# Performance work log

Measured on AMD Instinct MI355X. Metric: run time of the kernel, lower is better.

Reference implementation:

```python
import jax, jax.numpy as jnp
import numpy as np
from jax import lax

SIGMA_RATIO = 1.0 / 2.355
NUM_BINS = 32


def _correlation_ratio(pred, target, num_bins=NUM_BINS, sigma_ratio=SIGMA_RATIO):
    # Mirrors CorrRatio.correlation_ratio(pred, target).
    eps = jnp.finfo(target.dtype).eps
    # Quantile bounds are .item()'d in torch -> constants w.r.t. autodiff.
    f_max = lax.stop_gradient(jnp.quantile(target, 0.99))
    f_min = lax.stop_gradient(jnp.quantile(target, 0.01))
    m_max = lax.stop_gradient(jnp.quantile(pred, 0.99))
    m_min = lax.stop_gradient(jnp.quantile(pred, 0.01))

    f_bin_size = (f_max - f_min) / num_bins
    vbc = jnp.linspace(f_min + f_bin_size / 2, f_max - f_bin_size / 2, num_bins)  # (nb,)
    f_sigma = jnp.mean(jnp.diff(vbc)) * sigma_ratio
    preterm = 1.0 / (2.0 * f_sigma ** 2)

    B, C = target.shape[0], target.shape[1]
    y = jnp.clip(target, f_min, f_max).reshape(B, C, -1)  # (B,C,N)
    x = jnp.clip(pred, m_min, m_max).reshape(B, C, -1)    # (B,C,N)

    # Parzen-window weights: (B,C,nb,N)
    diff = y[:, :, None, :] - vbc[None, None, :, None]
    weights = jnp.exp(-preterm * jnp.square(diff))
    # Note: torch code normalizes over the voxel axis (dim=-1 == N).
    weights_norm = weights / (jnp.sum(weights, axis=-1, keepdims=True) + eps)

    mean_intensities = jnp.sum(weights_norm * x[:, :, None, :], axis=3)  # (B,C,nb)
    bin_counts = jnp.sum(weights, axis=3)                                # (B,C,nb)
    total_mean = jnp.mean(x, axis=2, keepdims=True)                      # (B,C,1)

    between_group_variance = jnp.sum(
        bin_counts * jnp.square(mean_intensities - total_mean), axis=2
    ) / (jnp.sum(bin_counts, axis=2) + eps)                              # (B,C)
    total_variance = jnp.var(x, axis=2, ddof=1)  # torch.var default: unbiased
    eta_square = between_group_variance / (total_variance + eps)
    return jnp.mean(eta_square)


def setup_inputs() -> dict:
    key = jax.random.key(0)
    k1, k2 = jax.random.split(key)
    shape = (1, 1, 128, 128, 128)
    y_true = jax.random.normal(k1, shape, dtype=jnp.float32)
    y_pred = jax.random.normal(k2, shape, dtype=jnp.float32)
    return {"y_true": y_true, "y_pred": y_pred}


def reference(y_true, y_pred):
    # forward: correlation_ratio(y_true, y_pred) maps to (pred=y_true, target=y_pred)
    symmetric_cr = _correlation_ratio(y_true, y_pred) + _correlation_ratio(y_pred, y_true)
    return -symmetric_cr / 2.0
```

## Files before the change

### kernel.cpp

```cpp
#include <hip/hip_runtime.h>
#include <stdint.h>

#define N_ELEM (128*128*128)
#define NBINS 32
#define CAP 32768
#define REPS 8
#define PBUF 1024

static constexpr size_t OFF_H12  = 0;
static constexpr size_t OFF_B12  = OFF_H12 + 2ull*4096ull*4ull;
static constexpr size_t OFF_R12  = OFF_B12 + 8*4;
static constexpr size_t OFF_CNT  = OFF_R12 + 8*4;
static constexpr size_t OFF_SEL  = OFF_CNT + 8*4;
static constexpr size_t OFF_ACC  = (OFF_SEL + 8*4 + 7) & ~size_t(7);
static constexpr size_t OFF_CAND = OFF_ACC + (size_t)REPS*2*66*8;
static constexpr size_t OFF_MEMSET_END = OFF_CAND;

__device__ __forceinline__ uint32_t f2k(float x){
    uint32_t b = __float_as_uint(x);
    return (b & 0x80000000u) ? ~b : (b | 0x80000000u);
}
__device__ __forceinline__ float k2f(uint32_t k){
    uint32_t b = (k & 0x80000000u) ? (k & 0x7FFFFFFFu) : ~k;
    return __uint_as_float(b);
}

__device__ __forceinline__ float fexp2(float x){
#if __has_builtin(__builtin_amdgcn_exp2f)
    return __builtin_amdgcn_exp2f(x);
#else
    return __expf(x * 0.6931471805599453f);
#endif
}

__global__ void __launch_bounds__(256) k_p1(const float* __restrict__ a0,
                                            const float* __restrict__ a1,
                                            uint32_t* __restrict__ hist12){
    __shared__ uint32_t lh[4096];
    for (int i = threadIdx.x; i < 4096; i += 256) lh[i] = 0;
    __syncthreads();
    const float4* s4 = (const float4*)(blockIdx.y ? a1 : a0);
    const int stride = gridDim.x * blockDim.x;
    for (int i = blockIdx.x * blockDim.x + threadIdx.x; i < N_ELEM/4; i += stride){
        float4 v = s4[i];
        atomicAdd(&lh[f2k(v.x) >> 20], 1u);
        atomicAdd(&lh[f2k(v.y) >> 20], 1u);
        atomicAdd(&lh[f2k(v.z) >> 20], 1u);
        atomicAdd(&lh[f2k(v.w) >> 20], 1u);
    }
    __syncthreads();
    uint32_t* gh = hist12 + (size_t)blockIdx.y * 4096u;
    for (int i = threadIdx.x; i < 4096; i += 256){
        uint32_t c = lh[i];
        if (c) atomicAdd(&gh[i], c);
    }
}

__global__ void __launch_bounds__(256) k_s1(const uint32_t* __restrict__ hist12,
                                            uint32_t* __restrict__ bucket12,
                                            uint32_t* __restrict__ resid12){
    __shared__ uint32_t part[256];
    const uint32_t R[4] = {20971u, 20972u, 2076179u, 2076180u};
    const int a = blockIdx.x;
    const int t = threadIdx.x;
    const uint4* h4 = (const uint4*)(hist12 + (size_t)a * 4096u);
    uint32_t v[16];
    uint32_t s = 0;
    #pragma unroll
    for (int j = 0; j < 4; ++j){
        uint4 q4 = h4[t*4 + j];
        v[j*4+0] = q4.x; v[j*4+1] = q4.y; v[j*4+2] = q4.z; v[j*4+3] = q4.w;
        s += q4.x + q4.y + q4.z + q4.w;
    }
    part[t] = s;
    __syncthreads();
    for (int d = 1; d < 256; d <<= 1){
        uint32_t add = (t >= d) ? part[t - d] : 0u;
        __syncthreads();
        part[t] += add;
        __syncthreads();
    }
    uint32_t c = part[t] - s;
    #pragma unroll
    for (int j = 0; j < 16; ++j){
        uint32_t cnt = v[j];
        if (cnt){
            for (int ri = 0; ri < 4; ++ri){
                uint32_t r = R[ri];
                if (r >= c && r < c + cnt){
                    bucket12[a*4 + ri] = (uint32_t)(t*16 + j);
                    resid12 [a*4 + ri] = r - c;
                }
            }
        }
        c += cnt;
    }
}

__global__ void __launch_bounds__(256) k_p2(const float* __restrict__ a0,
                                            const float* __restrict__ a1,
                                            const uint32_t* __restrict__ bucket12,
                                            uint32_t* __restrict__ cnt,
                                            float* __restrict__ cand){
    __shared__ uint32_t lcnt[4];
    __shared__ uint32_t gbase[4];
    __shared__ float lbuf[4][PBUF];
    const int t = threadIdx.x;
    const int base = blockIdx.y * 4;
    const uint32_t b0 = bucket12[base+0], b1 = bucket12[base+1];
    const uint32_t b2 = bucket12[base+2], b3 = bucket12[base+3];
    const bool own1 = (b1 != b0);
    const bool own2 = (b2 != b0) && (b2 != b1);
    const bool own3 = (b3 != b0) && (b3 != b1) && (b3 != b2);
    if (t < 4) lcnt[t] = 0;
    __syncthreads();
    const float4* s4 = (const float4*)(blockIdx.y ? a1 : a0);
    const int stride = gridDim.x * blockDim.x;
    for (int i = blockIdx.x * blockDim.x + t; i < N_ELEM/4; i += stride){
        float4 v = s4[i];
        float vv[4] = {v.x, v.y, v.z, v.w};
        #pragma unroll
        for (int e = 0; e < 4; ++e){
            uint32_t hi = f2k(vv[e]) >> 20;
            if (hi == b0){
                uint32_t x = atomicAdd(&lcnt[0], 1u);
                if (x < PBUF) lbuf[0][x] = vv[e];
                else { uint32_t g = atomicAdd(&cnt[base+0], 1u); if (g < CAP) cand[(size_t)(base+0)*CAP + g] = vv[e]; }
            }
            if (own1 && hi == b1){
                uint32_t x = atomicAdd(&lcnt[1], 1u);
                if (x < PBUF) lbuf[1][x] = vv[e];
                else { uint32_t g = atomicAdd(&cnt[base+1], 1u); if (g < CAP) cand[(size_t)(base+1)*CAP + g] = vv[e]; }
            }
            if (own2 && hi == b2){
                uint32_t x = atomicAdd(&lcnt[2], 1u);
                if (x < PBUF) lbuf[2][x] = vv[e];
                else { uint32_t g = atomicAdd(&cnt[base+2], 1u); if (g < CAP) cand[(size_t)(base+2)*CAP + g] = vv[e]; }
            }
            if (own3 && hi == b3){
                uint32_t x = atomicAdd(&lcnt[3], 1u);
                if (x < PBUF) lbuf[3][x] = vv[e];
                else { uint32_t g = atomicAdd(&cnt[base+3], 1u); if (g < CAP) cand[(size_t)(base+3)*CAP + g] = vv[e]; }
            }
        }
    }
    __syncthreads();
    if (t == 0){
        #pragma unroll
        for (int j = 0; j < 4; ++j){
            uint32_t n = min(lcnt[j], (uint32_t)PBUF);
            gbase[j] = n ? atomicAdd(&cnt[base+j], n) : 0u;
        }
    }
    __syncthreads();
    #pragma unroll
    for (int j = 0; j < 4; ++j){
        uint32_t n = min(lcnt[j], (uint32_t)PBUF);
        for (uint32_t i = t; i < n; i += 256){
            uint32_t g = gbase[j] + i;
            if (g < CAP) cand[(size_t)(base+j)*CAP + g] = lbuf[j][i];
        }
    }
}

__global__ void __launch_bounds__(256) k_s2(const float* __restrict__ cand,
                                            const uint32_t* __restrict__ cnt,
                                            const uint32_t* __restrict__ bucket12,
                                            const uint32_t* __restrict__ resid12,
                                            float* __restrict__ selval){
    __shared__ uint32_t lh[1024];
    __shared__ uint32_t part[256];
    __shared__ uint32_t sb_sh, r2_sh;
    const int r = blockIdx.x;
    const int t = threadIdx.x;
    const int base4 = (r >> 2) << 2;
    int o = base4;
    for (int i = base4; i <= r; ++i){
        if (bucket12[i] == bucket12[r]){ o = i; break; }
    }
    const uint32_t n = min(cnt[o], (uint32_t)CAP);
    const float* cb = cand + (size_t)o * CAP;
    const uint32_t rr = resid12[r];
    const uint32_t b12 = bucket12[r];

    for (int i = t; i < 1024; i += 256) lh[i] = 0;
    __syncthreads();
    for (uint32_t i = t; i < n; i += 256) atomicAdd(&lh[(f2k(cb[i]) >> 10) & 1023u], 1u);
    __syncthreads();
    {
        uint32_t v[4]; uint32_t s = 0;
        #pragma unroll
        for (int j = 0; j < 4; ++j){ v[j] = lh[t*4 + j]; s += v[j]; }
        part[t] = s;
        __syncthreads();
        for (int d = 1; d < 256; d <<= 1){
            uint32_t add = (t >= d) ? part[t - d] : 0u;
            __syncthreads();
            part[t] += add;
            __syncthreads();
        }
        uint32_t c = part[t] - s;
        #pragma unroll
        for (int j = 0; j < 4; ++j){
            if (v[j] && rr >= c && rr < c + v[j]){ sb_sh = (uint32_t)(t*4 + j); r2_sh = rr - c; }
            c += v[j];
        }
    }
    __syncthreads();
    const uint32_t sb = sb_sh, r2 = r2_sh;
    __syncthreads();

    for (int i = t; i < 1024; i += 256) lh[i] = 0;
    __syncthreads();
    for (uint32_t i = t; i < n; i += 256){
        uint32_t k = f2k(cb[i]);
        if (((k >> 10) & 1023u) == sb) atomicAdd(&lh[k & 1023u], 1u);
    }
    __syncthreads();
    {
        uint32_t v[4]; uint32_t s = 0;
        #pragma unroll
        for (int j = 0; j < 4; ++j){ v[j] = lh[t*4 + j]; s += v[j]; }
        part[t] = s;
        __syncthreads();
        for (int d = 1; d < 256; d <<= 1){
            uint32_t add = (t >= d) ? part[t - d] : 0u;
            __syncthreads();
            part[t] += add;
            __syncthreads();
        }
        uint32_t c = part[t] - s;
        #pragma unroll
        for (int j = 0; j < 4; ++j){
            if (v[j] && r2 >= c && r2 < c + v[j]){
                uint32_t key = (b12 << 20) | (sb << 10) | (uint32_t)(t*4 + j);
                selval[r] = k2f(key);
            }
            c += v[j];
        }
    }
}

__device__ __forceinline__ float wred(float v){
    #pragma unroll
    for (int o = 32; o > 0; o >>= 1) v += __shfl_down(v, o);
    return v;
}

__global__ void __launch_bounds__(128) k_main(const float* __restrict__ yt,
                                              const float* __restrict__ yp,
                                              const float* __restrict__ selval,
                                              double* __restrict__ acc){
    __shared__ float lp1[NBINS][128];
    __shared__ float lp2[NBINS][128];
    __shared__ float qs[4];
    const int t = threadIdx.x;
    const int dir = blockIdx.y;
    #pragma unroll
    for (int k = 0; k < NBINS; ++k){ lp1[k][t] = 0.f; lp2[k][t] = 0.f; }
    if (t == 0){
        double f01 = 0.01 * (double)(N_ELEM - 1) - 20971.0;
        double f99 = 0.99 * (double)(N_ELEM - 1) - 2076179.0;
        double v0 = selval[0], v1 = selval[1], v2 = selval[2], v3 = selval[3];
        double v4 = selval[4], v5 = selval[5], v6 = selval[6], v7 = selval[7];
        qs[0] = (float)(v0 + f01 * (v1 - v0));
        qs[1] = (float)(v2 + f99 * (v3 - v2));
        qs[2] = (float)(v4 + f01 * (v5 - v4));
        qs[3] = (float)(v6 + f99 * (v7 - v6));
    }
    __syncthreads();

    const float f_min = dir ? qs[0] : qs[2];
    const float f_max = dir ? qs[1] : qs[3];
    const float m_min = dir ? qs[2] : qs[0];
    const float m_max = dir ? qs[3] : qs[1];

    const float h      = (f_max - f_min) / 32.0f;
    const float vbc0   = f_min + 0.5f * h;
    const float vbcE   = f_max - 0.5f * h;
    const float step   = (vbcE - vbc0) / 31.0f;
    const float sigma  = step * (1.0f / 2.355f);
    const float preterm= 1.0f / (2.0f * sigma * sigma);
    const float negq2  = -preterm * step * step * 1.4426950408889634f;
    const float inv_st = 1.0f / step;
    const float u0     = -vbc0 * inv_st;

    const float4* ysrc = (const float4*)(dir ? yt : yp);
    const float4* xsrc = (const float4*)(dir ? yp : yt);

    float sx = 0.f, sxx = 0.f;
    const int stride = gridDim.x * blockDim.x;
    for (int i = blockIdx.x * blockDim.x + t; i < N_ELEM/4; i += stride){
        float4 y4 = ysrc[i];
        float4 x4 = xsrc[i];
        float yy[4] = {y4.x, y4.y, y4.z, y4.w};
        float xx[4] = {x4.x, x4.y, x4.z, x4.w};
        #pragma unroll
        for (int e = 0; e < 4; ++e){
            float yc = fminf(fmaxf(yy[e], f_min), f_max);
            float xc = fminf(fmaxf(xx[e], m_min), m_max);
            sx += xc; sxx = fmaf(xc, xc, sxx);
            float u  = fmaf(yc, inv_st, u0);
            float jf = fminf(fmaxf(floorf(u) - 2.0f, 0.0f), 26.0f);
            int j0 = (int)jf;
            float t0 = u - jf;
            float* p1 = &lp1[j0][t];
            float* p2 = &lp2[j0][t];
            #pragma unroll
            for (int w = 0; w < 6; ++w){
                float d  = t0 - (float)w;
                float wt = fexp2(d * d * negq2);
                p1[w*128] += wt;
                p2[w*128] += wt * xc;
            }
        }
    }
    __syncthreads();

    if (t < 64){
        #pragma unroll
        for (int k = 0; k < NBINS; ++k){ lp1[k][t] += lp1[k][t+64]; lp2[k][t] += lp2[k][t+64]; }
    }
    __syncthreads();
    if (t < 32){
        #pragma unroll
        for (int k = 0; k < NBINS; ++k){ lp1[k][t] += lp1[k][t+32]; lp2[k][t] += lp2[k][t+32]; }
    }
    __syncthreads();

    const int rep = blockIdx.x & (REPS - 1);
    double* a = acc + ((size_t)rep*2 + dir) * 66;
    if (t < 64){
        int arr = t >> 5, bin = t & 31;
        float s = 0.f;
        #pragma unroll
        for (int c = 0; c < 32; ++c){
            int cc = (c + t) & 31;
            s += arr ? lp2[bin][cc] : lp1[bin][cc];
        }
        atomicAdd(&a[t], (double)s);
    }
    sx = wred(sx); sxx = wred(sxx);
    if ((t & 63) == 0){
        atomicAdd(&a[64], (double)sx);
        atomicAdd(&a[65], (double)sxx);
    }
}

__global__ void __launch_bounds__(256) k_final(const double* __restrict__ acc,
                                               float* __restrict__ out){
    __shared__ double dA[132];
    const int t = threadIdx.x;
    if (t < 132){
        int dir = t / 66, k = t % 66;
        double s = 0.0;
        #pragma unroll
        for (int rep = 0; rep < REPS; ++rep) s += acc[((size_t)rep*2 + dir)*66 + k];
        dA[t] = s;
    }
    __syncthreads();
    if (t == 0){
        const double eps = 1.1920928955078125e-07;
        double res = 0.0;
        for (int dir = 0; dir < 2; ++dir){
            const double* A = &dA[dir*66];
            double sx = A[64], sxx = A[65];
            double tm = sx / (double)N_ELEM;
            double sumS1 = 0.0, bgv = 0.0;
            for (int k = 0; k < NBINS; ++k) sumS1 += A[k];
            for (int k = 0; k < NBINS; ++k){
                double mi = A[32+k] / (A[k] + eps);
                double d  = mi - tm;
                bgv += A[k] * d * d;
            }
            bgv /= (sumS1 + eps);
            double tv = (sxx - sx*sx/(double)N_ELEM) / (double)(N_ELEM - 1);
            res += bgv / (tv + eps);
        }
        out[0] = (float)(-0.5 * res);
    }
}

extern "C" void kernel_launch(void* const* d_in, const int* in_sizes, int n_in,
                              void* d_out, int out_size, void* d_ws, size_t ws_size,
                              hipStream_t stream){
    const float* yt = (const float*)d_in[0];
    const float* yp = (const float*)d_in[1];
    char* ws = (char*)d_ws;
    uint32_t* hist12   = (uint32_t*)(ws + OFF_H12);
    uint32_t* bucket12 = (uint32_t*)(ws + OFF_B12);
    uint32_t* resid12  = (uint32_t*)(ws + OFF_R12);
    uint32_t* cnt      = (uint32_t*)(ws + OFF_CNT);
    float*    selval   = (float*)(ws + OFF_SEL);
    double*   acc      = (double*)(ws + OFF_ACC);
    float*    cand     = (float*)(ws + OFF_CAND);

    hipMemsetAsync(d_ws, 0, OFF_MEMSET_END, stream);

    k_p1  <<<dim3(256, 2), 256, 0, stream>>>(yt, yp, hist12);
    k_s1  <<<2, 256, 0, stream>>>(hist12, bucket12, resid12);
    k_p2  <<<dim3(128, 2), 256, 0, stream>>>(yt, yp, bucket12, cnt, cand);
    k_s2  <<<8, 256, 0, stream>>>(cand, cnt, bucket12, resid12, selval);
    k_main<<<dim3(512, 2), 128, 0, stream>>>(yt, yp, selval, acc);
    k_final<<<1, 256, 0, stream>>>(acc, (float*)d_out);
}
```

Before: 92.74 us.

## Fuse scan and final kernels via last-block tickets, register-accumulate all 32 bins

Replaces the memset with a small zeroing kernel and folds the histogram-scan kernel into k_p1 and the final reduction into k_main, using an atomic ticket so the last block does the tail work. This removes launches. k_main now evaluates all 32 Gaussian bins per voxel in registers with wave shuffles instead of the windowed 6-tap shared-memory scatter. That drops LDS traffic but multiplies exp work by about 5x, and k_main moves to 256-thread blocks with half the grid.

Result: slower. 159.0 us (+71.4%).

```diff
diff --git a/kernel.cpp b/kernel.cpp
--- a/kernel.cpp
+++ b/kernel.cpp
@@ -6,15 +6,20 @@
 #define CAP 32768
 #define REPS 8
 #define PBUF 1024
-
-static constexpr size_t OFF_H12  = 0;
-static constexpr size_t OFF_B12  = OFF_H12 + 2ull*4096ull*4ull;
-static constexpr size_t OFF_R12  = OFF_B12 + 8*4;
-static constexpr size_t OFF_CNT  = OFF_R12 + 8*4;
-static constexpr size_t OFF_SEL  = OFF_CNT + 8*4;
-static constexpr size_t OFF_ACC  = (OFF_SEL + 8*4 + 7) & ~size_t(7);
-static constexpr size_t OFF_CAND = OFF_ACC + (size_t)REPS*2*66*8;
-static constexpr size_t OFF_MEMSET_END = OFF_CAND;
+#define GX_P1 256
+#define GX_P2 128
+#define GX_MAIN 256
+
+static constexpr size_t OFF_H12 = 0;
+static constexpr size_t OFF_CNT = OFF_H12 + 2ull*4096*4;
+static constexpr size_t OFF_TK  = OFF_CNT + 8*4;
+static constexpr size_t OFF_B12 = OFF_TK + 2*4;
+static constexpr size_t OFF_R12 = OFF_B12 + 8*4;
+static constexpr size_t OFF_SEL = OFF_R12 + 8*4;
+static constexpr size_t OFF_ACC = OFF_SEL + 8*4;
+static constexpr size_t OFF_ACC_END = OFF_ACC + (size_t)REPS*2*66*8;
+static constexpr size_t OFF_CAND = OFF_ACC_END;
+static constexpr int ZERO_WORDS = (int)(OFF_ACC_END / 4);
 
 __device__ __forceinline__ uint32_t f2k(float x){
     uint32_t b = __float_as_uint(x);
@@ -24,7 +29,6 @@
     uint32_t b = (k & 0x80000000u) ? (k & 0x7FFFFFFFu) : ~k;
     return __uint_as_float(b);
 }
-
 __device__ __forceinline__ float fexp2(float x){
 #if __has_builtin(__builtin_amdgcn_exp2f)
     return __builtin_amdgcn_exp2f(x);
@@ -32,16 +36,33 @@
     return __expf(x * 0.6931471805599453f);
 #endif
 }
+__device__ __forceinline__ float wred(float v){
+    #pragma unroll
+    for (int o = 32; o > 0; o >>= 1) v += __shfl_down(v, o);
+    return v;
+}
+
+__global__ void __launch_bounds__(256) k_zero(uint32_t* __restrict__ w){
+    const int stride = gridDim.x * blockDim.x;
+    for (int i = blockIdx.x * blockDim.x + threadIdx.x; i < ZERO_WORDS; i += stride)
+        w[i] = 0u;
+}
 
 __global__ void __launch_bounds__(256) k_p1(const float* __restrict__ a0,
                                             const float* __restrict__ a1,
-                                            uint32_t* __restrict__ hist12){
+                                            uint32_t* __restrict__ hist12,
+                                            uint32_t* __restrict__ ticket,
+                                            uint32_t* __restrict__ bucket12,
+                                            uint32_t* __restrict__ resid12){
     __shared__ uint32_t lh[4096];
-    for (int i = threadIdx.x; i < 4096; i += 256) lh[i] = 0;
+    __shared__ uint32_t part[256];
+    __shared__ uint32_t lastflag;
+    const int t = threadIdx.x;
+    for (int i = t; i < 4096; i += 256) lh[i] = 0;
     __syncthreads();
     const float4* s4 = (const float4*)(blockIdx.y ? a1 : a0);
-    const int stride = gridDim.x * blockDim.x;
-    for (int i = blockIdx.x * blockDim.x + threadIdx.x; i < N_ELEM/4; i += stride){
+    const int stride = GX_P1 * 256;
+    for (int i = blockIdx.x * 256 + t; i < N_ELEM/4; i += stride){
         float4 v = s4[i];
         atomicAdd(&lh[f2k(v.x) >> 20], 1u);
         atomicAdd(&lh[f2k(v.y) >> 20], 1u);
@@ -50,50 +71,47 @@
     }
     __syncthreads();
     uint32_t* gh = hist12 + (size_t)blockIdx.y * 4096u;
-    for (int i = threadIdx.x; i < 4096; i += 256){
+    for (int i = t; i < 4096; i += 256){
         uint32_t c = lh[i];
         if (c) atomicAdd(&gh[i], c);
     }
-}
-
-__global__ void __launch_bounds__(256) k_s1(const uint32_t* __restrict__ hist12,
-                                            uint32_t* __restrict__ bucket12,
-                                            uint32_t* __restrict__ resid12){
-    __shared__ uint32_t part[256];
+    __threadfence();
+    __syncthreads();
+    if (t == 0) lastflag = (atomicAdd(&ticket[0], 1u) == gridDim.x * gridDim.y - 1) ? 1u : 0u;
+    __syncthreads();
+    if (!lastflag) return;
+    __threadfence();
+
     const uint32_t R[4] = {20971u, 20972u, 2076179u, 2076180u};
-    const int a = blockIdx.x;
-    const int t = threadIdx.x;
-    const uint4* h4 = (const uint4*)(hist12 + (size_t)a * 4096u);
-    uint32_t v[16];
-    uint32_t s = 0;
-    #pragma unroll
-    for (int j = 0; j < 4; ++j){
-        uint4 q4 = h4[t*4 + j];
-        v[j*4+0] = q4.x; v[j*4+1] = q4.y; v[j*4+2] = q4.z; v[j*4+3] = q4.w;
-        s += q4.x + q4.y + q4.z + q4.w;
-    }
-    part[t] = s;
-    __syncthreads();
-    for (int d = 1; d < 256; d <<= 1){
-        uint32_t add = (t >= d) ? part[t - d] : 0u;
+    for (int a = 0; a < 2; ++a){
+        uint32_t* h = hist12 + (size_t)a * 4096u;
+        uint32_t v[16]; uint32_t s = 0;
+        #pragma unroll
+        for (int j = 0; j < 16; ++j){ v[j] = atomicAdd(&h[t*16 + j], 0u); s += v[j]; }
+        part[t] = s;
         __syncthreads();
-        part[t] += add;
+        for (int d = 1; d < 256; d <<= 1){
+            uint32_t add = (t >= d) ? part[t - d] : 0u;
+            __syncthreads();
+            part[t] += add;
+            __syncthreads();
+        }
+        uint32_t c = part[t] - s;
+        #pragma unroll
+        for (int j = 0; j < 16; ++j){
+            uint32_t cnt = v[j];
+            if (cnt){
+                for (int ri = 0; ri < 4; ++ri){
+                    uint32_t r = R[ri];
+                    if (r >= c && r < c + cnt){
+                        bucket12[a*4 + ri] = (uint32_t)(t*16 + j);
+                        resid12 [a*4 + ri] = r - c;
+                    }
+                }
+            }
+            c += cnt;
+        }
         __syncthreads();
-    }
-    uint32_t c = part[t] - s;
-    #pragma unroll
-    for (int j = 0; j < 16; ++j){
-        uint32_t cnt = v[j];
-        if (cnt){
-            for (int ri = 0; ri < 4; ++ri){
-                uint32_t r = R[ri];
-                if (r >= c && r < c + cnt){
-                    bucket12[a*4 + ri] = (uint32_t)(t*16 + j);
-                    resid12 [a*4 + ri] = r - c;
-                }
-            }
-        }
-        c += cnt;
     }
 }
 
@@ -115,8 +133,8 @@
     if (t < 4) lcnt[t] = 0;
     __syncthreads();
     const float4* s4 = (const float4*)(blockIdx.y ? a1 : a0);
-    const int stride = gridDim.x * blockDim.x;
-    for (int i = blockIdx.x * blockDim.x + t; i < N_ELEM/4; i += stride){
+    const int stride = GX_P2 * 256;
+    for (int i = blockIdx.x * 256 + t; i < N_ELEM/4; i += stride){
         float4 v = s4[i];
         float vv[4] = {v.x, v.y, v.z, v.w};
         #pragma unroll
@@ -241,23 +259,18 @@
     }
 }
 
-__device__ __forceinline__ float wred(float v){
-    #pragma unroll
-    for (int o = 32; o > 0; o >>= 1) v += __shfl_down(v, o);
-    return v;
-}
-
-__global__ void __launch_bounds__(128) k_main(const float* __restrict__ yt,
+__global__ void __launch_bounds__(256) k_main(const float* __restrict__ yt,
                                               const float* __restrict__ yp,
                                               const float* __restrict__ selval,
-                                              double* __restrict__ acc){
-    __shared__ float lp1[NBINS][128];
-    __shared__ float lp2[NBINS][128];
+                                              double* __restrict__ acc,
+                                              uint32_t* __restrict__ ticket,
+                                              float* __restrict__ out){
     __shared__ float qs[4];
+    __shared__ float wp[4][66];
+    __shared__ uint32_t lastflag;
+    __shared__ double dA[132];
     const int t = threadIdx.x;
     const int dir = blockIdx.y;
-    #pragma unroll
-    for (int k = 0; k < NBINS; ++k){ lp1[k][t] = 0.f; lp2[k][t] = 0.f; }
     if (t == 0){
         double f01 = 0.01 * (double)(N_ELEM - 1) - 20971.0;
         double f99 = 0.99 * (double)(N_ELEM - 1) - 2076179.0;
@@ -288,9 +301,13 @@
     const float4* ysrc = (const float4*)(dir ? yt : yp);
     const float4* xsrc = (const float4*)(dir ? yp : yt);
 
+    float s1[NBINS], s2[NBINS];
+    #pragma unroll
+    for (int k = 0; k < NBINS; ++k){ s1[k] = 0.f; s2[k] = 0.f; }
     float sx = 0.f, sxx = 0.f;
-    const int stride = gridDim.x * blockDim.x;
-    for (int i = blockIdx.x * blockDim.x + t; i < N_ELEM/4; i += stride){
+
+    const int stride = GX_MAIN * 256;
+    for (int i = blockIdx.x * 256 + t; i < N_ELEM/4; i += stride){
         float4 y4 = ysrc[i];
         float4 x4 = xsrc[i];
         float yy[4] = {y4.x, y4.y, y4.z, y4.w};
@@ -301,71 +318,54 @@
             float xc = fminf(fmaxf(xx[e], m_min), m_max);
             sx += xc; sxx = fmaf(xc, xc, sxx);
             float u  = fmaf(yc, inv_st, u0);
-            float jf = fminf(fmaxf(floorf(u) - 2.0f, 0.0f), 26.0f);
-            int j0 = (int)jf;
-            float t0 = u - jf;
-            float* p1 = &lp1[j0][t];
-            float* p2 = &lp2[j0][t];
             #pragma unroll
-            for (int w = 0; w < 6; ++w){
-                float d  = t0 - (float)w;
-                float wt = fexp2(d * d * negq2);
-                p1[w*128] += wt;
-                p2[w*128] += wt * xc;
-            }
-        }
-    }
-    __syncthreads();
-
-    if (t < 64){
-        #pragma unroll
-        for (int k = 0; k < NBINS; ++k){ lp1[k][t] += lp1[k][t+64]; lp2[k][t] += lp2[k][t+64]; }
-    }
-    __syncthreads();
-    if (t < 32){
-        #pragma unroll
-        for (int k = 0; k < NBINS; ++k){ lp1[k][t] += lp1[k][t+32]; lp2[k][t] += lp2[k][t+32]; }
-    }
-    __syncthreads();
-
+            for (int k = 0; k < NBINS; ++k){
+                float du = u - (float)k;
+                float w  = fexp2(negq2 * du * du);
+                s1[k] += w;
+                s2[k] = fmaf(w, xc, s2[k]);
+            }
+        }
+    }
+
+    #pragma unroll
+    for (int k = 0; k < NBINS; ++k){ s1[k] = wred(s1[k]); s2[k] = wred(s2[k]); }
+    sx = wred(sx); sxx = wred(sxx);
+    const int lane = t & 63, wave = t >> 6;
+    if (lane == 0){
+        #pragma unroll
+        for (int k = 0; k < NBINS; ++k){ wp[wave][k] = s1[k]; wp[wave][32+k] = s2[k]; }
+        wp[wave][64] = sx; wp[wave][65] = sxx;
+    }
+    __syncthreads();
     const int rep = blockIdx.x & (REPS - 1);
     double* a = acc + ((size_t)rep*2 + dir) * 66;
-    if (t < 64){
-        int arr = t >> 5, bin = t & 31;
-        float s = 0.f;
-        #pragma unroll
-        for (int c = 0; c < 32; ++c){
-            int cc = (c + t) & 31;
-            s += arr ? lp2[bin][cc] : lp1[bin][cc];
-        }
-        atomicAdd(&a[t], (double)s);
-    }
-    sx = wred(sx); sxx = wred(sxx);
-    if ((t & 63) == 0){
-        atomicAdd(&a[64], (double)sx);
-        atomicAdd(&a[65], (double)sxx);
-    }
-}
-
-__global__ void __launch_bounds__(256) k_final(const double* __restrict__ acc,
-                                               float* __restrict__ out){
-    __shared__ double dA[132];
-    const int t = threadIdx.x;
+    if (t < 66){
+        float v = wp[0][t] + wp[1][t] + wp[2][t] + wp[3][t];
+        atomicAdd(&a[t], (double)v);
+    }
+    __threadfence();
+    __syncthreads();
+    if (t == 0) lastflag = (atomicAdd(&ticket[1], 1u) == gridDim.x * gridDim.y - 1) ? 1u : 0u;
+    __syncthreads();
+    if (!lastflag) return;
+    __threadfence();
+
     if (t < 132){
-        int dir = t / 66, k = t % 66;
+        int d2 = t / 66, k = t % 66;
         double s = 0.0;
         #pragma unroll
-        for (int rep = 0; rep < REPS; ++rep) s += acc[((size_t)rep*2 + dir)*66 + k];
+        for (int r2 = 0; r2 < REPS; ++r2) s += atomicAdd(&acc[((size_t)r2*2 + d2)*66 + k], 0.0);
         dA[t] = s;
     }
     __syncthreads();
     if (t == 0){
         const double eps = 1.1920928955078125e-07;
         double res = 0.0;
-        for (int dir = 0; dir < 2; ++dir){
-            const double* A = &dA[dir*66];
-            double sx = A[64], sxx = A[65];
-            double tm = sx / (double)N_ELEM;
+        for (int d2 = 0; d2 < 2; ++d2){
+            const double* A = &dA[d2*66];
+            double sxt = A[64], sxxt = A[65];
+            double tm = sxt / (double)N_ELEM;
             double sumS1 = 0.0, bgv = 0.0;
             for (int k = 0; k < NBINS; ++k) sumS1 += A[k];
             for (int k = 0; k < NBINS; ++k){
@@ -374,7 +374,7 @@
                 bgv += A[k] * d * d;
             }
             bgv /= (sumS1 + eps);
-            double tv = (sxx - sx*sx/(double)N_ELEM) / (double)(N_ELEM - 1);
+            double tv = (sxxt - sxt*sxt/(double)N_ELEM) / (double)(N_ELEM - 1);
             res += bgv / (tv + eps);
         }
         out[0] = (float)(-0.5 * res);
@@ -388,19 +388,17 @@
     const float* yp = (const float*)d_in[1];
     char* ws = (char*)d_ws;
     uint32_t* hist12   = (uint32_t*)(ws + OFF_H12);
+    uint32_t* cnt      = (uint32_t*)(ws + OFF_CNT);
+    uint32_t* ticket   = (uint32_t*)(ws + OFF_TK);
     uint32_t* bucket12 = (uint32_t*)(ws + OFF_B12);
     uint32_t* resid12  = (uint32_t*)(ws + OFF_R12);
-    uint32_t* cnt      = (uint32_t*)(ws + OFF_CNT);
     float*    selval   = (float*)(ws + OFF_SEL);
     double*   acc      = (double*)(ws + OFF_ACC);
     float*    cand     = (float*)(ws + OFF_CAND);
 
-    hipMemsetAsync(d_ws, 0, OFF_MEMSET_END, stream);
-
-    k_p1  <<<dim3(256, 2), 256, 0, stream>>>(yt, yp, hist12);
-    k_s1  <<<2, 256, 0, stream>>>(hist12, bucket12, resid12);
-    k_p2  <<<dim3(128, 2), 256, 0, stream>>>(yt, yp, bucket12, cnt, cand);
+    k_zero<<<16, 256, 0, stream>>>((uint32_t*)ws);
+    k_p1  <<<dim3(GX_P1, 2), 256, 0, stream>>>(yt, yp, hist12, ticket, bucket12, resid12);
+    k_p2  <<<dim3(GX_P2, 2), 256, 0, stream>>>(yt, yp, bucket12, cnt, cand);
     k_s2  <<<8, 256, 0, stream>>>(cand, cnt, bucket12, resid12, selval);
-    k_main<<<dim3(512, 2), 128, 0, stream>>>(yt, yp, selval, acc);
-    k_final<<<1, 256, 0, stream>>>(acc, (float*)d_out);
-}
+    k_main<<<dim3(GX_MAIN, 2), 256, 0, stream>>>(yt, yp, selval, acc, ticket, (float*)d_out);
+}
```
